# Kernel tuning notes

Hardware: AMD Instinct MI355X
Metric: run time of the kernel (lower is better)

Reference implementation:

```python
import jax, jax.numpy as jnp
import numpy as np

B = 8192      # batch of matchups
L = 40        # history_len
HN = 32       # hist_numeric_dim
TE = 96       # team_embed_dim
SE = 32       # seed_embed_dim
HH = 64       # hist_hidden_dim
NH = 4        # num_heads
HD = HH // NH # head dim = 16
MID = 128     # middle_dim
BOX = 8       # box_score_dim
NT = 400      # num_teams
NS = 17       # num_seeds
TOWER_IN = TE + SE + 1 + 2 * HH  # 257
MERGED = 2 * MID                 # 256
EPS = 1e-5


def setup_inputs() -> dict:
    key = jax.random.key(0)
    ks = iter(jax.random.split(key, 80))
    nrm = lambda shape, s=0.05: (jax.random.normal(next(ks), shape, jnp.float32) * s)
    inp = {}
    inp['teamA_id'] = jax.random.randint(next(ks), (B,), 1, NT)
    inp['teamB_id'] = jax.random.randint(next(ks), (B,), 1, NT)
    inp['teamA_seed'] = jax.random.randint(next(ks), (B,), 0, NS)
    inp['teamB_seed'] = jax.random.randint(next(ks), (B,), 0, NS)
    inp['teamA_elo'] = 1500.0 + 200.0 * jax.random.normal(next(ks), (B,), jnp.float32)
    inp['teamB_elo'] = 1500.0 + 200.0 * jax.random.normal(next(ks), (B,), jnp.float32)
    inp['teamA_hist_numeric'] = jax.random.normal(next(ks), (B, L, HN), jnp.float32)
    inp['teamB_hist_numeric'] = jax.random.normal(next(ks), (B, L, HN), jnp.float32)
    inp['teamA_hist_opp_ids'] = jax.random.randint(next(ks), (B, L), 0, NT)
    inp['teamB_hist_opp_ids'] = jax.random.randint(next(ks), (B, L), 0, NT)
    # 0/1 padding mask; guarantee at least one valid game per row
    inp['teamA_hist_mask'] = (jax.random.uniform(next(ks), (B, L)) < 0.8).astype(jnp.float32).at[:, 0].set(1.0)
    inp['teamB_hist_mask'] = (jax.random.uniform(next(ks), (B, L)) < 0.8).astype(jnp.float32).at[:, 0].set(1.0)
    # parameters
    inp['team_emb'] = nrm((NT, TE), 0.1).at[0].set(0.0)  # padding_idx=0
    inp['seed_emb'] = nrm((NS, SE), 0.1)
    inp['conv_w'] = nrm((HH, HN + TE, 3))
    inp['conv_b'] = nrm((HH,))
    inp['cbn_g'] = jnp.ones((HH,)); inp['cbn_b'] = jnp.zeros((HH,))
    inp['cbn_rm'] = nrm((HH,), 0.01); inp['cbn_rv'] = jnp.ones((HH,))
    inp['hp_w'] = nrm((HH, HN + TE)); inp['hp_b'] = nrm((HH,))
    inp['qp_w'] = nrm((HH, TE)); inp['qp_b'] = nrm((HH,))
    inp['attn_in_w'] = nrm((3 * HH, HH)); inp['attn_in_b'] = nrm((3 * HH,))
    inp['attn_out_w'] = nrm((HH, HH)); inp['attn_out_b'] = nrm((HH,))
    inp['ln_g'] = jnp.ones((HH,)); inp['ln_b'] = jnp.zeros((HH,))
    inp['tw_w'] = nrm((MID, TOWER_IN)); inp['tw_b'] = nrm((MID,))
    inp['tbn_g'] = jnp.ones((MID,)); inp['tbn_b'] = jnp.zeros((MID,))
    inp['tbn_rm'] = nrm((MID,), 0.01); inp['tbn_rv'] = jnp.ones((MID,))
    inp['r1_w'] = nrm((MERGED, MERGED)); inp['r1_b'] = nrm((MERGED,))
    inp['r1bn_g'] = jnp.ones((MERGED,)); inp['r1bn_b'] = jnp.zeros((MERGED,))
    inp['r1bn_rm'] = nrm((MERGED,), 0.01); inp['r1bn_rv'] = jnp.ones((MERGED,))
    inp['r2_w'] = nrm((MERGED, MERGED)); inp['r2_b'] = nrm((MERGED,))
    inp['r2bn_g'] = jnp.ones((MERGED,)); inp['r2bn_b'] = jnp.zeros((MERGED,))
    inp['r2bn_rm'] = nrm((MERGED,), 0.01); inp['r2bn_rv'] = jnp.ones((MERGED,))
    inp['mu_w'] = nrm((BOX, MERGED)); inp['mu_b'] = nrm((BOX,))
    inp['lv_w'] = nrm((BOX, MERGED)); inp['lv_b'] = nrm((BOX,))
    inp['wl_w'] = nrm((1, MERGED)); inp['wl_b'] = nrm((1,))
    return inp


def _bn(x, g, b, rm, rv):
    # eval-mode BatchNorm over last axis
    return (x - rm) * jax.lax.rsqrt(rv + EPS) * g + b


def _ln(x, g, b):
    m = jnp.mean(x, axis=-1, keepdims=True)
    v = jnp.var(x, axis=-1, keepdims=True)
    return (x - m) * jax.lax.rsqrt(v + EPS) * g + b


def reference(teamA_id, teamB_id, teamA_seed, teamB_seed, teamA_elo, teamB_elo,
              teamA_hist_numeric, teamA_hist_opp_ids, teamA_hist_mask,
              teamB_hist_numeric, teamB_hist_opp_ids, teamB_hist_mask,
              team_emb, seed_emb, conv_w, conv_b, cbn_g, cbn_b, cbn_rm, cbn_rv,
              hp_w, hp_b, qp_w, qp_b, attn_in_w, attn_in_b, attn_out_w, attn_out_b,
              ln_g, ln_b, tw_w, tw_b, tbn_g, tbn_b, tbn_rm, tbn_rv,
              r1_w, r1_b, r1bn_g, r1bn_b, r1bn_rm, r1bn_rv,
              r2_w, r2_b, r2bn_g, r2bn_b, r2bn_rm, r2bn_rv,
              mu_w, mu_b, lv_w, lv_b, wl_w, wl_b):
    silu = jax.nn.silu

    def attend(q_emb, hn, opp, mask):
        m = mask[..., None]
        x = jnp.concatenate([hn * m, team_emb[opp] * m], axis=-1)      # [B,L,HN+TE]
        res = silu(x @ hp_w.T + hp_b)                                   # [B,L,HH]
        c = jax.lax.conv_general_dilated(
            x.transpose(0, 2, 1), conv_w, (1,), [(1, 1)],
            dimension_numbers=('NCH', 'OIH', 'NCH')) + conv_b[:, None]  # [B,HH,L]
        c = _bn(c.transpose(0, 2, 1), cbn_g, cbn_b, cbn_rm, cbn_rv)     # [B,L,HH]
        kv = silu(c + res)                                              # [B,L,HH]
        q = q_emb @ qp_w.T + qp_b                                       # [B,HH]
        wq, wk, wv = jnp.split(attn_in_w, 3, axis=0)
        bq, bk, bv = jnp.split(attn_in_b, 3, axis=0)
        qh = (q @ wq.T + bq).reshape(-1, NH, HD)
        kh = (kv @ wk.T + bk).reshape(-1, L, NH, HD)
        vh = (kv @ wv.T + bv).reshape(-1, L, NH, HD)
        scores = jnp.einsum('bhd,blhd->bhl', qh, kh) / np.float32(np.sqrt(HD))
        scores = jnp.where(mask[:, None, :] > 0.0, scores, -1e9)
        a = jax.nn.softmax(scores, axis=-1)
        o = jnp.einsum('bhl,blhd->bhd', a, vh).reshape(-1, HH)
        o = o @ attn_out_w.T + attn_out_b
        return _ln(o + q, ln_g, ln_b)

    ea = team_emb[teamA_id]
    eb = team_emb[teamB_id]
    sa = seed_emb[teamA_seed]
    sb = seed_emb[teamB_seed]
    za = (teamA_elo[:, None] - 1500.0) / 400.0
    zb = (teamB_elo[:, None] - 1500.0) / 400.0

    aa = attend(ea, teamA_hist_numeric, teamA_hist_opp_ids, teamA_hist_mask)
    ab = attend(ea, teamB_hist_numeric, teamB_hist_opp_ids, teamB_hist_mask)
    bb = attend(eb, teamB_hist_numeric, teamB_hist_opp_ids, teamB_hist_mask)
    ba = attend(eb, teamA_hist_numeric, teamA_hist_opp_ids, teamA_hist_mask)

    ta = jnp.concatenate([ea, sa, za, aa, ab], axis=-1)
    tb = jnp.concatenate([eb, sb, zb, bb, ba], axis=-1)

    tower = lambda t: silu(_bn(t @ tw_w.T + tw_b, tbn_g, tbn_b, tbn_rm, tbn_rv))
    ra = tower(ta)
    rb = tower(tb)

    x = jnp.concatenate([ra - rb, ra * rb], axis=-1)
    x = silu(_bn(x @ r1_w.T + r1_b, r1bn_g, r1bn_b, r1bn_rm, r1bn_rv)) + x
    x = silu(_bn(x @ r2_w.T + r2_b, r2bn_g, r2bn_b, r2bn_rm, r2bn_rv)) + x

    box_mu = x @ mu_w.T + mu_b
    box_log_var = x @ lv_w.T + lv_b
    win_logit = (x @ wl_w.T + wl_b)[:, 0]
    return ((box_mu, box_log_var), win_logit)
```

## Files before the change

kernel.cpp:

```cpp
#include <hip/hip_runtime.h>
#include <stdint.h>

#define EPS 1e-5f

typedef __attribute__((ext_vector_type(8))) short short8;
typedef __attribute__((ext_vector_type(4))) float floatx4;
typedef __attribute__((ext_vector_type(4))) unsigned uintx4;
typedef unsigned short u16;

__device__ __forceinline__ u16 f2bf(float f) {
  unsigned u = __builtin_bit_cast(unsigned, f);
  u += 0x7fffu + ((u >> 16) & 1u);
  return (u16)(u >> 16);
}
__device__ __forceinline__ float bf2f(u16 h) {
  return __builtin_bit_cast(float, (unsigned)h << 16);
}
__device__ __forceinline__ unsigned pack2bf(float a, float b) {
  return (unsigned)f2bf(a) | ((unsigned)f2bf(b) << 16);
}
__device__ __forceinline__ float silu_f(float x) { return x / (1.f + __expf(-x)); }
__device__ __forceinline__ float wave_sum(float x) {
  for (int off = 32; off > 0; off >>= 1) x += __shfl_xor(x, off);
  return x;
}

__global__ void prep_kernel(const float* __restrict__ hp_w, const float* __restrict__ conv_w,
                            const float* __restrict__ attn_in_w,
                            const float* __restrict__ attn_out_w,
                            const float* __restrict__ tw_w, const float* __restrict__ r1_w,
                            const float* __restrict__ r2_w,
                            u16* __restrict__ w1f, u16* __restrict__ w2f,
                            float* __restrict__ woT,
                            float* __restrict__ twT, float* __restrict__ r1T,
                            float* __restrict__ r2T) {
  int t = blockIdx.x * 256 + threadIdx.x;
  if (t < 32768) {
    int j = t & 7, lane = (t >> 3) & 63, ks = (t >> 9) & 3, nt = t >> 11;
    int k = ks * 32 + ((lane >> 4) << 3) + j;
    int n = nt * 16 + (lane & 15);
    float v = (n < 64) ? hp_w[n * 128 + k]
                       : conv_w[((n - 64) & 63) * 384 + k * 3 + ((n - 64) >> 6)];
    w1f[t] = f2bf(v);
  }
  if (t < 8192) {
    int j = t & 7, lane = (t >> 3) & 63, ks = (t >> 9) & 1, nt = t >> 10;
    int k = ks * 32 + ((lane >> 4) << 3) + j;
    int n = nt * 16 + (lane & 15);
    w2f[t] = f2bf(attn_in_w[(64 + n) * 64 + k]);
  }
  if (t < 4096) {
    int j = t & 63, k = t >> 6;
    woT[k * 64 + j] = attn_out_w[j * 64 + k];
  }
  if (t < 8320) {
    int mid = t & 127, k4 = t >> 7;
#pragma unroll
    for (int i = 0; i < 4; ++i) {
      int k = k4 * 4 + i;
      twT[t * 4 + i] = (k < 257) ? tw_w[mid * 257 + k] : 0.f;
    }
  }
  if (t < 16384) {
    int o = t & 255, k4 = t >> 8;
#pragma unroll
    for (int i = 0; i < 4; ++i) {
      r1T[t * 4 + i] = r1_w[o * 256 + k4 * 4 + i];
      r2T[t * 4 + i] = r2_w[o * 256 + k4 * 4 + i];
    }
  }
}

__global__ __launch_bounds__(64) void team_kernel(
    const float* __restrict__ temb, const float* __restrict__ qp_w,
    const float* __restrict__ qp_b, const float* __restrict__ attn_in_w,
    const float* __restrict__ attn_in_b,
    float* __restrict__ Qg, float* __restrict__ QHg) {
  __shared__ float e[96];
  __shared__ float qv[64];
  const int t = blockIdx.x;
  const int o = threadIdx.x;
  for (int i = o; i < 96; i += 64) e[i] = temb[t * 96 + i];
  __syncthreads();
  float acc = qp_b[o];
  for (int k = 0; k < 96; ++k) acc += e[k] * qp_w[o * 96 + k];
  qv[o] = acc;
  Qg[t * 64 + o] = acc;
  __syncthreads();
  float acc2 = attn_in_b[o];
  for (int k = 0; k < 64; ++k) acc2 += qv[k] * attn_in_w[o * 64 + k];
  QHg[t * 64 + o] = acc2;
}

__global__ __launch_bounds__(256, 2) void attn_kernel(
    const int* __restrict__ idA, const int* __restrict__ idB,
    const float* __restrict__ hnA, const float* __restrict__ hnB,
    const int* __restrict__ oppA, const int* __restrict__ oppB,
    const float* __restrict__ mskA, const float* __restrict__ mskB,
    const float* __restrict__ temb, const float* __restrict__ conv_b,
    const float* __restrict__ cbn_g, const float* __restrict__ cbn_b,
    const float* __restrict__ cbn_rm, const float* __restrict__ cbn_rv,
    const float* __restrict__ hp_b,
    const float* __restrict__ attn_in_b, const float* __restrict__ attn_out_b,
    const float* __restrict__ ln_g, const float* __restrict__ ln_b,
    const u16* __restrict__ w1f, const u16* __restrict__ w2f,
    const float* __restrict__ woT,
    const float* __restrict__ Qg, const float* __restrict__ QHg,
    float* __restrict__ ATT) {
  __shared__ __align__(16) u16 xb[48 * 136];
  __shared__ __align__(16) u16 ybuf[48 * 264];
  __shared__ __align__(16) u16 kvb[48 * 72];
  __shared__ float a_s[8][40];
  __shared__ float o_s[2][64];
  __shared__ float qh_s[2][64];
  float* KVP = (float*)ybuf;

  const int tid = threadIdx.x;
  const int lane = tid & 63;
  const int wv = tid >> 6;
  const int qd = lane >> 4;
  const int l16 = lane & 15;

  const int c2 = (tid & 31) * 2;
  const int lb = tid >> 5;
  const float pw_sc0 = rsqrtf(cbn_rv[c2] + EPS) * cbn_g[c2];
  const float pw_sc1 = rsqrtf(cbn_rv[c2 + 1] + EPS) * cbn_g[c2 + 1];
  const float pw_sh0 = cbn_b[c2] - cbn_rm[c2] * pw_sc0;
  const float pw_sh1 = cbn_b[c2 + 1] - cbn_rm[c2 + 1] * pw_sc1;
  const float pw_hpb0 = hp_b[c2], pw_hpb1 = hp_b[c2 + 1];
  const float pw_cvb0 = conv_b[c2], pw_cvb1 = conv_b[c2 + 1];
  const float lng = ln_g[lane], lnb = ln_b[lane];
  const float aob = attn_out_b[lane];
  const float kb0 = attn_in_b[64 + (wv * 2 + 0) * 16 + l16];
  const float kb1 = attn_in_b[64 + (wv * 2 + 1) * 16 + l16];

  for (int idx = tid; idx < 8 * 64; idx += 256)
    kvb[(40 + (idx >> 6)) * 72 + (idx & 63)] = 0;
  __syncthreads();

  unsigned xr[12];
  float mkr[3];
  {
    int np = blockIdx.x;
    int pb = np >> 1;
    const float* phn = (np & 1) ? hnB : hnA;
    const int* popp = (np & 1) ? oppB : oppA;
    const float* pmsk = (np & 1) ? mskB : mskA;
#pragma unroll
    for (int j = 0; j < 3; ++j) {
      int sidx = j * 256 + tid;
      int srow = sidx >> 4, scg = sidx & 15;
      if (srow < 40) {
        int mrow = pb * 40 + srow;
        mkr[j] = pmsk[mrow];
        const float* p = (scg < 4)
                             ? phn + (size_t)mrow * 32 + scg * 8
                             : temb + (size_t)popp[mrow] * 96 + (scg * 8 - 32);
        floatx4 f0 = *reinterpret_cast<const floatx4*>(p);
        floatx4 f1 = *reinterpret_cast<const floatx4*>(p + 4);
        xr[j * 4 + 0] = pack2bf(f0[0], f0[1]);
        xr[j * 4 + 1] = pack2bf(f0[2], f0[3]);
        xr[j * 4 + 2] = pack2bf(f1[0], f1[1]);
        xr[j * 4 + 3] = pack2bf(f1[2], f1[3]);
      } else {
        mkr[j] = 0.f;
        xr[j * 4 + 0] = xr[j * 4 + 1] = xr[j * 4 + 2] = xr[j * 4 + 3] = 0u;
      }
    }
  }

#pragma unroll 1
  for (int it = 0; it < 8; ++it) {
    int pair = blockIdx.x + it * 2048;
    int b = pair >> 1, s = pair & 1;

#pragma unroll
    for (int j = 0; j < 3; ++j) {
      int sidx = j * 256 + tid;
      bool keep = mkr[j] != 0.f;
      uintx4 v;
      v[0] = keep ? xr[j * 4 + 0] : 0u;
      v[1] = keep ? xr[j * 4 + 1] : 0u;
      v[2] = keep ? xr[j * 4 + 2] : 0u;
      v[3] = keep ? xr[j * 4 + 3] : 0u;
      *reinterpret_cast<uintx4*>(xb + (sidx >> 4) * 136 + (sidx & 15) * 8) = v;
    }
    float qreg = 0.f, qhreg = 0.f, m_l = 0.f;
    if (wv < 2) {
      int id = wv ? idB[b] : idA[b];
      qreg = Qg[id * 64 + lane];
      qhreg = QHg[id * 64 + lane];
      if (lane < 40) m_l = (s ? mskB : mskA)[b * 40 + lane];
    }
    __syncthreads();

    {
      short8 af[3][4];
#pragma unroll
      for (int mt = 0; mt < 3; ++mt)
#pragma unroll
        for (int ks = 0; ks < 4; ++ks)
          af[mt][ks] = *reinterpret_cast<const short8*>(
              xb + (mt * 16 + l16) * 136 + ks * 32 + (qd << 3));
#pragma unroll 1
      for (int ntl = 0; ntl < 4; ++ntl) {
        short8 w[4];
#pragma unroll
        for (int ks = 0; ks < 4; ++ks)
          w[ks] = *reinterpret_cast<const short8*>(
              w1f + (((wv * 4 + ntl) * 4 + ks) * 64 + lane) * 8);
        floatx4 acc[3] = {};
#pragma unroll
        for (int ks = 0; ks < 4; ++ks)
#pragma unroll
          for (int mt = 0; mt < 3; ++mt)
            acc[mt] = __builtin_amdgcn_mfma_f32_16x16x32_bf16(
                af[mt][ks], w[ks], acc[mt], 0, 0, 0);
        int col = (wv * 4 + ntl) * 16 + l16;
#pragma unroll
        for (int mt = 0; mt < 3; ++mt)
#pragma unroll
          for (int r = 0; r < 4; ++r)
            ybuf[(mt * 16 + qd * 4 + r) * 264 + col] = f2bf(acc[mt][r]);
      }
    }
    __syncthreads();

    float pf[3][8];
    float mknew[3];
    short8 bf2[2][2];
    {
      int np = (it < 7) ? pair + 2048 : pair;
      int pb = np >> 1;
      const float* phn = (np & 1) ? hnB : hnA;
      const int* popp = (np & 1) ? oppB : oppA;
      const float* pmsk = (np & 1) ? mskB : mskA;
#pragma unroll
      for (int j = 0; j < 3; ++j) {
        int sidx = j * 256 + tid;
        int srow = sidx >> 4, scg = sidx & 15;
        if (srow < 40) {
          int mrow = pb * 40 + srow;
          mknew[j] = pmsk[mrow];
          const float* p = (scg < 4)
                               ? phn + (size_t)mrow * 32 + scg * 8
                               : temb + (size_t)popp[mrow] * 96 + (scg * 8 - 32);
          *reinterpret_cast<floatx4*>(&pf[j][0]) = *reinterpret_cast<const floatx4*>(p);
          *reinterpret_cast<floatx4*>(&pf[j][4]) = *reinterpret_cast<const floatx4*>(p + 4);
        } else {
          mknew[j] = 0.f;
#pragma unroll
          for (int q = 0; q < 8; ++q) pf[j][q] = 0.f;
        }
      }
#pragma unroll
      for (int ntl = 0; ntl < 2; ++ntl)
#pragma unroll
        for (int ks = 0; ks < 2; ++ks)
          bf2[ntl][ks] = *reinterpret_cast<const short8*>(
              w2f + (((wv * 2 + ntl) * 2 + ks) * 64 + lane) * 8);
    }

#pragma unroll
    for (int t = 0; t < 5; ++t) {
      int l = lb + 8 * t;
      unsigned yhp = *reinterpret_cast<const unsigned*>(ybuf + l * 264 + c2);
      unsigned t0 = (l >= 1) ? *reinterpret_cast<const unsigned*>(ybuf + (l - 1) * 264 + 64 + c2) : 0u;
      unsigned t1 = *reinterpret_cast<const unsigned*>(ybuf + l * 264 + 128 + c2);
      unsigned t2 = *reinterpret_cast<const unsigned*>(ybuf + (l + 1) * 264 + 192 + c2);
      float res0 = silu_f(bf2f((u16)yhp) + pw_hpb0);
      float res1 = silu_f(bf2f((u16)(yhp >> 16)) + pw_hpb1);
      float c0 = bf2f((u16)t0) + bf2f((u16)t1) + bf2f((u16)t2) + pw_cvb0;
      float c1 = bf2f((u16)(t0 >> 16)) + bf2f((u16)(t1 >> 16)) + bf2f((u16)(t2 >> 16)) + pw_cvb1;
      float kv0 = silu_f(c0 * pw_sc0 + pw_sh0 + res0);
      float kv1 = silu_f(c1 * pw_sc1 + pw_sh1 + res1);
      *reinterpret_cast<unsigned*>(kvb + l * 72 + c2) = pack2bf(kv0, kv1);
    }
    __syncthreads();

    {
      floatx4 acc[3][2] = {};
#pragma unroll
      for (int mt = 0; mt < 3; ++mt) {
        short8 af[2];
#pragma unroll
        for (int ks = 0; ks < 2; ++ks)
          af[ks] = *reinterpret_cast<const short8*>(
              kvb + (mt * 16 + l16) * 72 + ks * 32 + (qd << 3));
#pragma unroll
        for (int ntl = 0; ntl < 2; ++ntl)
#pragma unroll
          for (int ks = 0; ks < 2; ++ks)
            acc[mt][ntl] = __builtin_amdgcn_mfma_f32_16x16x32_bf16(
                af[ks], bf2[ntl][ks], acc[mt][ntl], 0, 0, 0);
      }
#pragma unroll
      for (int mt = 0; mt < 3; ++mt)
#pragma unroll
        for (int ntl = 0; ntl < 2; ++ntl)
#pragma unroll
          for (int r = 0; r < 4; ++r) {
            int row = mt * 16 + qd * 4 + r;
            int col = (wv * 2 + ntl) * 16 + l16;
            KVP[row * 129 + col] = acc[mt][ntl][r] + (ntl ? kb1 : kb0);
          }
    }
    __syncthreads();

#pragma unroll
    for (int j = 0; j < 3; ++j) {
      xr[j * 4 + 0] = pack2bf(pf[j][0], pf[j][1]);
      xr[j * 4 + 1] = pack2bf(pf[j][2], pf[j][3]);
      xr[j * 4 + 2] = pack2bf(pf[j][4], pf[j][5]);
      xr[j * 4 + 3] = pack2bf(pf[j][6], pf[j][7]);
      mkr[j] = mknew[j];
    }

    if (wv < 2) {
      int qi = wv;
      qh_s[qi][lane] = qhreg;
      float a[4];
#pragma unroll
      for (int h = 0; h < 4; ++h) {
        float e = 0.f;
        if (lane < 40 && m_l > 0.f) {
          float acc = 0.f;
#pragma unroll
          for (int d = 0; d < 16; ++d)
            acc += qh_s[qi][h * 16 + d] * KVP[lane * 129 + h * 16 + d];
          e = __expf(acc * 0.25f);
        }
        float sm = wave_sum(e);
        a[h] = e / sm;
      }
#pragma unroll
      for (int h = 0; h < 4; ++h)
        if (lane < 40) a_s[qi * 4 + h][lane] = a[h];
      {
        int p = qi * 4 + (lane >> 4);
        float acc = 0.f;
#pragma unroll 4
        for (int l = 0; l < 40; ++l) acc += a_s[p][l] * KVP[l * 129 + 64 + lane];
        o_s[qi][lane] = acc;
      }
      float r = aob + qreg;
#pragma unroll 4
      for (int k = 0; k < 64; ++k) r += o_s[qi][k] * woT[k * 64 + lane];
      float mean = wave_sum(r) * (1.f / 64.f);
      float dv = r - mean;
      float var = wave_sum(dv * dv) * (1.f / 64.f);
      float outv = dv * rsqrtf(var + EPS) * lng + lnb;
      ATT[((qi * 2 + s) * 8192 + b) * 64 + lane] = outv;
    }
  }
}

__global__ __launch_bounds__(256) void head_kernel(
    const int* __restrict__ idA, const int* __restrict__ idB,
    const int* __restrict__ seedA, const int* __restrict__ seedB,
    const float* __restrict__ eloA, const float* __restrict__ eloB,
    const float* __restrict__ temb, const float* __restrict__ semb,
    const float* __restrict__ twT, const float* __restrict__ tw_b,
    const float* __restrict__ tbn_g, const float* __restrict__ tbn_b,
    const float* __restrict__ tbn_rm, const float* __restrict__ tbn_rv,
    const float* __restrict__ r1T, const float* __restrict__ r1_b,
    const float* __restrict__ r1bn_g, const float* __restrict__ r1bn_b,
    const float* __restrict__ r1bn_rm, const float* __restrict__ r1bn_rv,
    const float* __restrict__ r2T, const float* __restrict__ r2_b,
    const float* __restrict__ r2bn_g, const float* __restrict__ r2bn_b,
    const float* __restrict__ r2bn_rm, const float* __restrict__ r2bn_rv,
    const float* __restrict__ mu_w, const float* __restrict__ mu_b,
    const float* __restrict__ lv_w, const float* __restrict__ lv_b,
    const float* __restrict__ wl_w, const float* __restrict__ wl_b,
    const float* __restrict__ ATT, float* __restrict__ out) {
  __shared__ __align__(16) float tv[2][8][260];
  __shared__ __align__(16) float rr[2][8][128];
  __shared__ __align__(16) float xv[8][256];
  __shared__ __align__(16) float xw[8][256];
  const int tid = threadIdx.x;
  const int b0 = blockIdx.x * 8;

  for (int idx = tid; idx < 2 * 8 * 260; idx += 256) {
    int k = idx % 260;
    int bi = (idx / 260) & 7;
    int team = idx / (260 * 8);
    int b = b0 + bi;
    float v;
    if (k < 96) v = temb[(team ? idB[b] : idA[b]) * 96 + k];
    else if (k < 128) v = semb[(team ? seedB[b] : seedA[b]) * 32 + (k - 96)];
    else if (k == 128) v = ((team ? eloB[b] : eloA[b]) - 1500.f) * (1.f / 400.f);
    else if (k < 193) v = ATT[((team * 2 + team) * 8192 + b) * 64 + (k - 129)];
    else if (k < 257) v = ATT[((team * 2 + (1 - team)) * 8192 + b) * 64 + (k - 193)];
    else v = 0.f;
    tv[team][bi][k] = v;
  }
  __syncthreads();

  {
    int team = tid >> 7, mid = tid & 127;
    const floatx4* twv = reinterpret_cast<const floatx4*>(twT);
    float acc[8];
#pragma unroll
    for (int bi = 0; bi < 8; ++bi) acc[bi] = tw_b[mid];
#pragma unroll 2
    for (int k4 = 0; k4 < 65; ++k4) {
      floatx4 w4 = twv[k4 * 128 + mid];
      floatx4 x4[8];
#pragma unroll
      for (int bi = 0; bi < 8; ++bi)
        x4[bi] = *reinterpret_cast<const floatx4*>(&tv[team][bi][k4 * 4]);
#pragma unroll
      for (int bi = 0; bi < 8; ++bi)
        acc[bi] += x4[bi][0] * w4[0] + x4[bi][1] * w4[1] +
                   x4[bi][2] * w4[2] + x4[bi][3] * w4[3];
    }
    float sc = rsqrtf(tbn_rv[mid] + EPS) * tbn_g[mid];
    float sh = tbn_b[mid] - tbn_rm[mid] * sc;
#pragma unroll
    for (int bi = 0; bi < 8; ++bi) rr[team][bi][mid] = silu_f(acc[bi] * sc + sh);
  }
  __syncthreads();
  {
    int o = tid;
#pragma unroll
    for (int bi = 0; bi < 8; ++bi)
      xv[bi][o] = (o < 128) ? (rr[0][bi][o] - rr[1][bi][o])
                            : (rr[0][bi][o - 128] * rr[1][bi][o - 128]);
  }
  __syncthreads();
  {
    int o = tid;
    const floatx4* r1v = reinterpret_cast<const floatx4*>(r1T);
    float acc[8];
#pragma unroll
    for (int bi = 0; bi < 8; ++bi) acc[bi] = r1_b[o];
#pragma unroll 2
    for (int k4 = 0; k4 < 64; ++k4) {
      floatx4 w4 = r1v[k4 * 256 + o];
      floatx4 x4[8];
#pragma unroll
      for (int bi = 0; bi < 8; ++bi)
        x4[bi] = *reinterpret_cast<const floatx4*>(&xv[bi][k4 * 4]);
#pragma unroll
      for (int bi = 0; bi < 8; ++bi)
        acc[bi] += x4[bi][0] * w4[0] + x4[bi][1] * w4[1] +
                   x4[bi][2] * w4[2] + x4[bi][3] * w4[3];
    }
    float sc = rsqrtf(r1bn_rv[o] + EPS) * r1bn_g[o];
    float sh = r1bn_b[o] - r1bn_rm[o] * sc;
#pragma unroll
    for (int bi = 0; bi < 8; ++bi) xw[bi][o] = silu_f(acc[bi] * sc + sh) + xv[bi][o];
  }
  __syncthreads();
  {
    int o = tid;
    const floatx4* r2v = reinterpret_cast<const floatx4*>(r2T);
    float acc[8];
#pragma unroll
    for (int bi = 0; bi < 8; ++bi) acc[bi] = r2_b[o];
#pragma unroll 2
    for (int k4 = 0; k4 < 64; ++k4) {
      floatx4 w4 = r2v[k4 * 256 + o];
      floatx4 x4[8];
#pragma unroll
      for (int bi = 0; bi < 8; ++bi)
        x4[bi] = *reinterpret_cast<const floatx4*>(&xw[bi][k4 * 4]);
#pragma unroll
      for (int bi = 0; bi < 8; ++bi)
        acc[bi] += x4[bi][0] * w4[0] + x4[bi][1] * w4[1] +
                   x4[bi][2] * w4[2] + x4[bi][3] * w4[3];
    }
    float sc = rsqrtf(r2bn_rv[o] + EPS) * r2bn_g[o];
    float sh = r2bn_b[o] - r2bn_rm[o] * sc;
#pragma unroll
    for (int bi = 0; bi < 8; ++bi) xv[bi][o] = silu_f(acc[bi] * sc + sh) + xw[bi][o];
  }
  __syncthreads();
  if (tid < 136) {
    int bi = tid / 17, j = tid % 17;
    const float* wrow = (j < 8) ? (mu_w + j * 256) : (j < 16) ? (lv_w + (j - 8) * 256) : wl_w;
    const floatx4* wrow4 = reinterpret_cast<const floatx4*>(wrow);
    float acc = (j < 8) ? mu_b[j] : (j < 16) ? lv_b[j - 8] : wl_b[0];
    for (int k4 = 0; k4 < 64; ++k4) {
      floatx4 x4 = *reinterpret_cast<const floatx4*>(&xv[bi][k4 * 4]);
      floatx4 w4 = wrow4[k4];
      acc += x4[0] * w4[0] + x4[1] * w4[1] + x4[2] * w4[2] + x4[3] * w4[3];
    }
    int b = b0 + bi;
    if (j < 8) out[b * 8 + j] = acc;
    else if (j < 16) out[65536 + b * 8 + (j - 8)] = acc;
    else out[131072 + b] = acc;
  }
}

extern "C" void kernel_launch(void* const* d_in, const int* in_sizes, int n_in,
                              void* d_out, int out_size, void* d_ws, size_t ws_size,
                              hipStream_t stream) {
  const int* idA = (const int*)d_in[0];
  const int* idB = (const int*)d_in[1];
  const int* seedA = (const int*)d_in[2];
  const int* seedB = (const int*)d_in[3];
  const float* eloA = (const float*)d_in[4];
  const float* eloB = (const float*)d_in[5];
  const float* hnA = (const float*)d_in[6];
  const float* hnB = (const float*)d_in[7];
  const int* oppA = (const int*)d_in[8];
  const int* oppB = (const int*)d_in[9];
  const float* mskA = (const float*)d_in[10];
  const float* mskB = (const float*)d_in[11];
  const float* temb = (const float*)d_in[12];
  const float* semb = (const float*)d_in[13];
  const float* conv_w = (const float*)d_in[14];
  const float* conv_b = (const float*)d_in[15];
  const float* cbn_g = (const float*)d_in[16];
  const float* cbn_b = (const float*)d_in[17];
  const float* cbn_rm = (const float*)d_in[18];
  const float* cbn_rv = (const float*)d_in[19];
  const float* hp_w = (const float*)d_in[20];
  const float* hp_b = (const float*)d_in[21];
  const float* qp_w = (const float*)d_in[22];
  const float* qp_b = (const float*)d_in[23];
  const float* attn_in_w = (const float*)d_in[24];
  const float* attn_in_b = (const float*)d_in[25];
  const float* attn_out_w = (const float*)d_in[26];
  const float* attn_out_b = (const float*)d_in[27];
  const float* ln_g = (const float*)d_in[28];
  const float* ln_b = (const float*)d_in[29];
  const float* tw_w = (const float*)d_in[30];
  const float* tw_b = (const float*)d_in[31];
  const float* tbn_g = (const float*)d_in[32];
  const float* tbn_b = (const float*)d_in[33];
  const float* tbn_rm = (const float*)d_in[34];
  const float* tbn_rv = (const float*)d_in[35];
  const float* r1_w = (const float*)d_in[36];
  const float* r1_b = (const float*)d_in[37];
  const float* r1bn_g = (const float*)d_in[38];
  const float* r1bn_b = (const float*)d_in[39];
  const float* r1bn_rm = (const float*)d_in[40];
  const float* r1bn_rv = (const float*)d_in[41];
  const float* r2_w = (const float*)d_in[42];
  const float* r2_b = (const float*)d_in[43];
  const float* r2bn_g = (const float*)d_in[44];
  const float* r2bn_b = (const float*)d_in[45];
  const float* r2bn_rm = (const float*)d_in[46];
  const float* r2bn_rv = (const float*)d_in[47];
  const float* mu_w = (const float*)d_in[48];
  const float* mu_b = (const float*)d_in[49];
  const float* lv_w = (const float*)d_in[50];
  const float* lv_b = (const float*)d_in[51];
  const float* wl_w = (const float*)d_in[52];
  const float* wl_b = (const float*)d_in[53];

  char* ws = (char*)d_ws;
  u16* w1f = (u16*)(ws + 0);
  u16* w2f = (u16*)(ws + 65536);
  float* woT = (float*)(ws + 81920);
  float* Qg = (float*)(ws + 98304);
  float* QHg = (float*)(ws + 200704);
  float* twT = (float*)(ws + 303104);
  float* r1T = (float*)(ws + 436224);
  float* r2T = (float*)(ws + 698368);
  float* ATT = (float*)(ws + 960512);

  prep_kernel<<<256, 256, 0, stream>>>(hp_w, conv_w, attn_in_w, attn_out_w,
                                       tw_w, r1_w, r2_w,
                                       w1f, w2f, woT, twT, r1T, r2T);
  team_kernel<<<400, 64, 0, stream>>>(temb, qp_w, qp_b, attn_in_w, attn_in_b, Qg, QHg);
  attn_kernel<<<2048, 256, 0, stream>>>(idA, idB, hnA, hnB, oppA, oppB, mskA, mskB,
                                        temb, conv_b, cbn_g, cbn_b, cbn_rm, cbn_rv,
                                        hp_b, attn_in_b, attn_out_b, ln_g, ln_b,
                                        w1f, w2f, woT, Qg, QHg, ATT);
  head_kernel<<<1024, 256, 0, stream>>>(idA, idB, seedA, seedB, eloA, eloB, temb, semb,
                                        twT, tw_b, tbn_g, tbn_b, tbn_rm, tbn_rv,
                                        r1T, r1_b, r1bn_g, r1bn_b, r1bn_rm, r1bn_rv,
                                        r2T, r2_b, r2bn_g, r2bn_b, r2bn_rm, r2bn_rv,
                                        mu_w, mu_b, lv_w, lv_b, wl_w, wl_b,
                                        ATT, (float*)d_out);
}
```

Before: 588.7 us.

## Hoist MFMA weight fragments into registers and vectorize attention output projection

Loads the conv/hist-projection and K/V projection weight fragments into registers once per block instead of reloading them from global memory every iteration. The first GEMM loop is reordered to iterate over row tiles with all four column tiles accumulated at once. The output-projection weights are repacked so each lane reads float4 chunks, and the small attention dot products use split accumulators to shorten dependency chains. Holding more weights in registers raises VGPR pressure and may reduce occupancy.

Result: no change. 581.9 us (-1.1%).

```diff
diff --git a/kernel.cpp b/kernel.cpp
--- a/kernel.cpp
+++ b/kernel.cpp
@@ -49,9 +49,11 @@
     int n = nt * 16 + (lane & 15);
     w2f[t] = f2bf(attn_in_w[(64 + n) * 64 + k]);
   }
-  if (t < 4096) {
-    int j = t & 63, k = t >> 6;
-    woT[k * 64 + j] = attn_out_w[j * 64 + k];
+  if (t < 1024) {
+    int j = t & 63, k4 = t >> 6;
+#pragma unroll
+    for (int i = 0; i < 4; ++i)
+      woT[(k4 * 64 + j) * 4 + i] = attn_out_w[j * 64 + k4 * 4 + i];
   }
   if (t < 8320) {
     int mid = t & 127, k4 = t >> 7;
@@ -111,7 +113,7 @@
   __shared__ __align__(16) u16 ybuf[48 * 264];
   __shared__ __align__(16) u16 kvb[48 * 72];
   __shared__ float a_s[8][40];
-  __shared__ float o_s[2][64];
+  __shared__ __align__(16) float o_s[2][64];
   __shared__ float qh_s[2][64];
   float* KVP = (float*)ybuf;
 
@@ -131,12 +133,25 @@
   const float pw_cvb0 = conv_b[c2], pw_cvb1 = conv_b[c2 + 1];
   const float lng = ln_g[lane], lnb = ln_b[lane];
   const float aob = attn_out_b[lane];
-  const float kb0 = attn_in_b[64 + (wv * 2 + 0) * 16 + l16];
-  const float kb1 = attn_in_b[64 + (wv * 2 + 1) * 16 + l16];
 
   for (int idx = tid; idx < 8 * 64; idx += 256)
     kvb[(40 + (idx >> 6)) * 72 + (idx & 63)] = 0;
   __syncthreads();
+
+  short8 w1r[4][4];
+#pragma unroll
+  for (int ntl = 0; ntl < 4; ++ntl)
+#pragma unroll
+    for (int ks = 0; ks < 4; ++ks)
+      w1r[ntl][ks] = *reinterpret_cast<const short8*>(
+          w1f + (((wv * 4 + ntl) * 4 + ks) * 64 + lane) * 8);
+  short8 w2r[2][2];
+#pragma unroll
+  for (int ntl = 0; ntl < 2; ++ntl)
+#pragma unroll
+    for (int ks = 0; ks < 2; ++ks)
+      w2r[ntl][ks] = *reinterpret_cast<const short8*>(
+          w2f + (((wv * 2 + ntl) * 2 + ks) * 64 + lane) * 8);
 
   unsigned xr[12];
   float mkr[3];
@@ -194,41 +209,31 @@
     }
     __syncthreads();
 
-    {
-      short8 af[3][4];
-#pragma unroll
-      for (int mt = 0; mt < 3; ++mt)
-#pragma unroll
-        for (int ks = 0; ks < 4; ++ks)
-          af[mt][ks] = *reinterpret_cast<const short8*>(
-              xb + (mt * 16 + l16) * 136 + ks * 32 + (qd << 3));
 #pragma unroll 1
-      for (int ntl = 0; ntl < 4; ++ntl) {
-        short8 w[4];
-#pragma unroll
-        for (int ks = 0; ks < 4; ++ks)
-          w[ks] = *reinterpret_cast<const short8*>(
-              w1f + (((wv * 4 + ntl) * 4 + ks) * 64 + lane) * 8);
-        floatx4 acc[3] = {};
-#pragma unroll
-        for (int ks = 0; ks < 4; ++ks)
-#pragma unroll
-          for (int mt = 0; mt < 3; ++mt)
-            acc[mt] = __builtin_amdgcn_mfma_f32_16x16x32_bf16(
-                af[mt][ks], w[ks], acc[mt], 0, 0, 0);
-        int col = (wv * 4 + ntl) * 16 + l16;
-#pragma unroll
-        for (int mt = 0; mt < 3; ++mt)
-#pragma unroll
-          for (int r = 0; r < 4; ++r)
-            ybuf[(mt * 16 + qd * 4 + r) * 264 + col] = f2bf(acc[mt][r]);
-      }
+    for (int mt = 0; mt < 3; ++mt) {
+      short8 af[4];
+#pragma unroll
+      for (int ks = 0; ks < 4; ++ks)
+        af[ks] = *reinterpret_cast<const short8*>(
+            xb + (mt * 16 + l16) * 136 + ks * 32 + (qd << 3));
+      floatx4 acc[4] = {};
+#pragma unroll
+      for (int ks = 0; ks < 4; ++ks)
+#pragma unroll
+        for (int ntl = 0; ntl < 4; ++ntl)
+          acc[ntl] = __builtin_amdgcn_mfma_f32_16x16x32_bf16(
+              af[ks], w1r[ntl][ks], acc[ntl], 0, 0, 0);
+#pragma unroll
+      for (int ntl = 0; ntl < 4; ++ntl)
+#pragma unroll
+        for (int r = 0; r < 4; ++r)
+          ybuf[(mt * 16 + qd * 4 + r) * 264 + (wv * 4 + ntl) * 16 + l16] =
+              f2bf(acc[ntl][r]);
     }
     __syncthreads();
 
     float pf[3][8];
     float mknew[3];
-    short8 bf2[2][2];
     {
       int np = (it < 7) ? pair + 2048 : pair;
       int pb = np >> 1;
@@ -253,12 +258,6 @@
           for (int q = 0; q < 8; ++q) pf[j][q] = 0.f;
         }
       }
-#pragma unroll
-      for (int ntl = 0; ntl < 2; ++ntl)
-#pragma unroll
-        for (int ks = 0; ks < 2; ++ks)
-          bf2[ntl][ks] = *reinterpret_cast<const short8*>(
-              w2f + (((wv * 2 + ntl) * 2 + ks) * 64 + lane) * 8);
     }
 
 #pragma unroll
@@ -279,6 +278,8 @@
     __syncthreads();
 
     {
+      const float kb0 = attn_in_b[64 + (wv * 2 + 0) * 16 + l16];
+      const float kb1 = attn_in_b[64 + (wv * 2 + 1) * 16 + l16];
       floatx4 acc[3][2] = {};
 #pragma unroll
       for (int mt = 0; mt < 3; ++mt) {
@@ -292,7 +293,7 @@
 #pragma unroll
           for (int ks = 0; ks < 2; ++ks)
             acc[mt][ntl] = __builtin_amdgcn_mfma_f32_16x16x32_bf16(
-                af[ks], bf2[ntl][ks], acc[mt][ntl], 0, 0, 0);
+                af[ks], w2r[ntl][ks], acc[mt][ntl], 0, 0, 0);
       }
 #pragma unroll
       for (int mt = 0; mt < 3; ++mt)
@@ -324,11 +325,13 @@
       for (int h = 0; h < 4; ++h) {
         float e = 0.f;
         if (lane < 40 && m_l > 0.f) {
-          float acc = 0.f;
-#pragma unroll
-          for (int d = 0; d < 16; ++d)
-            acc += qh_s[qi][h * 16 + d] * KVP[lane * 129 + h * 16 + d];
-          e = __expf(acc * 0.25f);
+          float s0 = 0.f, s1 = 0.f;
+#pragma unroll
+          for (int d = 0; d < 16; d += 2) {
+            s0 += qh_s[qi][h * 16 + d] * KVP[lane * 129 + h * 16 + d];
+            s1 += qh_s[qi][h * 16 + d + 1] * KVP[lane * 129 + h * 16 + d + 1];
+          }
+          e = __expf((s0 + s1) * 0.25f);
         }
         float sm = wave_sum(e);
         a[h] = e / sm;
@@ -338,14 +341,24 @@
         if (lane < 40) a_s[qi * 4 + h][lane] = a[h];
       {
         int p = qi * 4 + (lane >> 4);
-        float acc = 0.f;
-#pragma unroll 4
-        for (int l = 0; l < 40; ++l) acc += a_s[p][l] * KVP[l * 129 + 64 + lane];
-        o_s[qi][lane] = acc;
+        float v0 = 0.f, v1 = 0.f;
+#pragma unroll
+        for (int l = 0; l < 40; l += 2) {
+          v0 += a_s[p][l] * KVP[l * 129 + 64 + lane];
+          v1 += a_s[p][l + 1] * KVP[(l + 1) * 129 + 64 + lane];
+        }
+        o_s[qi][lane] = v0 + v1;
       }
-      float r = aob + qreg;
-#pragma unroll 4
-      for (int k = 0; k < 64; ++k) r += o_s[qi][k] * woT[k * 64 + lane];
+      float acc0 = aob + qreg, acc1 = 0.f;
+      const floatx4* wo4 = reinterpret_cast<const floatx4*>(woT);
+#pragma unroll 8
+      for (int k4 = 0; k4 < 16; ++k4) {
+        floatx4 w4 = wo4[k4 * 64 + lane];
+        floatx4 x4 = *reinterpret_cast<const floatx4*>(&o_s[qi][k4 * 4]);
+        acc0 += x4[0] * w4[0] + x4[2] * w4[2];
+        acc1 += x4[1] * w4[1] + x4[3] * w4[3];
+      }
+      float r = acc0 + acc1;
       float mean = wave_sum(r) * (1.f / 64.f);
       float dv = r - mean;
       float var = wave_sum(dv * dv) * (1.f / 64.f);
```
